# Optimization experiments

Hardware: AMD Instinct MI355X
Metric: run time of the kernel (lower is better)

## Reference

```python
import jax, jax.numpy as jnp
import numpy as np

NUM_HEADS = 8
ATTN_LEN = 5


def setup_inputs() -> dict:
    rng = jax.random.key(0)
    ks = jax.random.split(rng, 10)
    B, T, D = 2, 4096, 1024
    H, HD = NUM_HEADS, D // NUM_HEADS
    n = lambda k, shape, scale=1.0: jax.random.normal(k, shape, jnp.float32) * scale
    return {
        "query": n(ks[0], (B, T, D)),
        "key": n(ks[1], (B, T, D)),
        "value": n(ks[2], (B, T, D)),
        "Wq": n(ks[3], (D, D), 0.02),
        "bq": jnp.zeros((D,), jnp.float32),
        "Wk": n(ks[4], (D, D), 0.02),
        "bk": jnp.zeros((D,), jnp.float32),
        "Wv": n(ks[5], (D, D), 0.02),
        "bv": jnp.zeros((D,), jnp.float32),
        "Er": n(ks[6], (H, HD, ATTN_LEN)),
        "layer": 1,
    }


def _forward(query, key, value, Wq, bq, Wk, bk, Wv, bv, Er, layer):
    B, T, D = query.shape
    H = NUM_HEADS
    HD = D // H
    dil = 2 ** layer
    pad = dil * (ATTN_LEN // 2)
    Tp = T + 2 * pad

    # torch nn.Linear: y = x @ W^T + b ; reshape to [B, H, T, HD]
    q = (query @ Wq.T + bq).reshape(B, T, H, HD).transpose(0, 2, 1, 3)
    k = (key @ Wk.T + bk).reshape(B, T, H, HD).transpose(0, 2, 1, 3)
    v = (value @ Wv.T + bv).reshape(B, T, H, HD).transpose(0, 2, 1, 3)

    # head-group source mapping + shifts (note k head 7 reuses k head 6, per source)
    src_k = jnp.array([0, 1, 2, 3, 4, 5, 6, 6])
    src_v = jnp.array([0, 1, 2, 3, 4, 5, 6, 7])
    shifts = jnp.array([0, 0, 0, 0, -2, -1, 1, 2])

    # kv_roll equivalence: window slot j at time t for shift s reads
    # padded[(t + (s + j) * dil) mod Tp]  (torch.roll wraparound included)
    t_idx = jnp.arange(T)
    j_idx = jnp.arange(ATTN_LEN)
    idx = (t_idx[None, :, None] + (shifts[:, None, None] + j_idx[None, None, :]) * dil) % Tp  # [H,T,L]

    def windows(x, src):
        xp = jnp.pad(x, ((0, 0), (0, 0), (pad, pad), (0, 0)))[:, src]  # [B,H,Tp,HD]
        g = jnp.take_along_axis(xp, idx.reshape(1, H, T * ATTN_LEN, 1), axis=2)
        return g.reshape(B, H, T, ATTN_LEN, HD)

    kw = windows(k, src_k)  # [B,H,T,L,HD]
    vw = windows(v, src_v)

    qk = jnp.einsum('bhtd,bhtjd->bhtj', q, kw)            # [B,H,T,L]
    mask = jnp.where(qk == 0.0, -jnp.inf, 0.0)            # zero dot product => padding
    qer = jnp.einsum('bhtd,hdj->bhtj', q, Er)             # relative positional bias
    attn = jax.nn.softmax((qk + qer) / np.sqrt(HD).astype(np.float32) + mask, axis=-1)
    out = jnp.einsum('bhtj,bhtjd->bhtd', attn, vw)        # [B,H,T,HD]
    out = out.transpose(0, 2, 1, 3).reshape(B, T, D)
    return out, attn[:, :, :, None, :]                     # attn shaped [B,H,T,1,L] like torch


def reference(query, key, value, Wq, bq, Wk, bk, Wv, bv, Er, layer):
    return _forward(query, key, value, Wq, bq, Wk, bk, Wv, bv, Er, layer)
```

## Files before the change

kernel.cpp:

```cpp
#include <hip/hip_runtime.h>
#include <hip/hip_bf16.h>

constexpr int B_ = 2, T_ = 4096, D_ = 1024, H_ = 8, HD_ = 128, L_ = 5;
constexpr int M_ = B_ * T_;
constexpr int K_ = D_;
constexpr int N_ = D_;
constexpr int TB_ = 64;
constexpr int NSMAX_ = 96;

typedef __attribute__((ext_vector_type(8))) __bf16 bf16x8;
typedef __attribute__((ext_vector_type(4))) float f32x4;

__device__ __constant__ int c_srck[8]  = {0, 1, 2, 3, 4, 5, 6, 6};
__device__ __constant__ int c_shift[8] = {0, 0, 0, 0, -2, -1, 1, 2};

__device__ __forceinline__ void gload_lds16(const void* g, void* l) {
    __builtin_amdgcn_global_load_lds(
        (__attribute__((address_space(1))) void*)g,
        (__attribute__((address_space(3))) void*)l, 16, 0, 0);
}

__global__ __launch_bounds__(256) void cvt_kernel(
    const float* __restrict__ q,  const float* __restrict__ k,  const float* __restrict__ v,
    const float* __restrict__ wq, const float* __restrict__ wk, const float* __restrict__ wv,
    __hip_bfloat16* __restrict__ qb,  __hip_bfloat16* __restrict__ kb,  __hip_bfloat16* __restrict__ vb,
    __hip_bfloat16* __restrict__ wqb, __hip_bfloat16* __restrict__ wkb, __hip_bfloat16* __restrict__ wvb)
{
    const int y = blockIdx.y;
    const float* src;
    __hip_bfloat16* dst;
    size_t idx;
    if (blockIdx.x < 4096) {
        src = (y == 0) ? q : (y == 1) ? k : v;
        dst = (y == 0) ? qb : (y == 1) ? kb : vb;
        idx = ((size_t)blockIdx.x * 256 + threadIdx.x) * 8;
    } else {
        src = (y == 0) ? wq : (y == 1) ? wk : wv;
        dst = (y == 0) ? wqb : (y == 1) ? wkb : wvb;
        idx = ((size_t)(blockIdx.x - 4096) * 256 + threadIdx.x) * 8;
    }
    f32x4 a = *(const f32x4*)(const void*)(src + idx);
    f32x4 b = *(const f32x4*)(const void*)(src + idx + 4);
    bf16x8 o;
#pragma unroll
    for (int e = 0; e < 4; ++e) { o[e] = (__bf16)a[e]; o[e + 4] = (__bf16)b[e]; }
    *(bf16x8*)(void*)(dst + idx) = o;
}

__global__ __launch_bounds__(256) void qkv_gemm_bf16(
    const __hip_bfloat16* __restrict__ qb,
    const __hip_bfloat16* __restrict__ kb,
    const __hip_bfloat16* __restrict__ vb,
    const __hip_bfloat16* __restrict__ wqb,
    const __hip_bfloat16* __restrict__ wkb,
    const __hip_bfloat16* __restrict__ wvb,
    const float* __restrict__ bq,
    const float* __restrict__ bk,
    const float* __restrict__ bv,
    __hip_bfloat16* __restrict__ qout,
    __hip_bfloat16* __restrict__ kout,
    __hip_bfloat16* __restrict__ vout)
{
    const int z = blockIdx.z;
    const __hip_bfloat16* A = (z == 0) ? qb  : (z == 1) ? kb  : vb;
    const __hip_bfloat16* W = (z == 0) ? wqb : (z == 1) ? wkb : wvb;
    const float* bias       = (z == 0) ? bq  : (z == 1) ? bk  : bv;
    __hip_bfloat16* C       = (z == 0) ? qout : (z == 1) ? kout : vout;

    __shared__ __align__(16) __hip_bfloat16 As[128 * 32];
    __shared__ __align__(16) __hip_bfloat16 Bs[128 * 32];

    const int tid  = threadIdx.x;
    const int wave = tid >> 6;
    const int lane = tid & 63;
    const int m0 = blockIdx.x * 128;
    const int n0 = blockIdx.y * 128;
    const int wm = (wave >> 1) * 64;
    const int wn = (wave & 1) * 64;

    f32x4 acc[4][4];
#pragma unroll
    for (int i = 0; i < 4; ++i)
#pragma unroll
        for (int j = 0; j < 4; ++j)
            acc[i][j] = (f32x4){0.f, 0.f, 0.f, 0.f};

    const int srow = lane >> 2;
    const int scol = (lane & 3) * 8;

    const int fr = lane & 15;
    const int fk = (lane >> 4) * 8;

    for (int k0 = 0; k0 < K_; k0 += 32) {
#pragma unroll
        for (int r = 0; r < 2; ++r) {
            const int issue = wave + r * 4;
            const int row = issue * 16 + srow;
            gload_lds16(A + (size_t)(m0 + row) * K_ + k0 + scol,
                        (void*)(As + issue * 512));
            gload_lds16(W + (size_t)(n0 + row) * K_ + k0 + scol,
                        (void*)(Bs + issue * 512));
        }
        __syncthreads();

        bf16x8 af[4], bf[4];
#pragma unroll
        for (int i = 0; i < 4; ++i) {
            af[i] = *(const bf16x8*)(const void*)(As + (wm + i * 16 + fr) * 32 + fk);
            bf[i] = *(const bf16x8*)(const void*)(Bs + (wn + i * 16 + fr) * 32 + fk);
        }
#pragma unroll
        for (int i = 0; i < 4; ++i)
#pragma unroll
            for (int j = 0; j < 4; ++j)
                acc[i][j] = __builtin_amdgcn_mfma_f32_16x16x32_bf16(
                    af[i], bf[j], acc[i][j], 0, 0, 0);
        __syncthreads();
    }

    const int col_l = lane & 15;
    const int row_l = (lane >> 4) * 4;
#pragma unroll
    for (int j = 0; j < 4; ++j) {
        const int n = n0 + wn + j * 16 + col_l;
        const float bval = bias[n];
#pragma unroll
        for (int i = 0; i < 4; ++i) {
            const int m = m0 + wm + i * 16 + row_l;
#pragma unroll
            for (int r = 0; r < 4; ++r)
                C[(size_t)(m + r) * N_ + n] = __float2bfloat16(acc[i][j][r] + bval);
        }
    }
}

__global__ __launch_bounds__(256) void qkv_gemm_f32(
    const float* __restrict__ query,
    const float* __restrict__ key,
    const float* __restrict__ value,
    const float* __restrict__ Wq,
    const float* __restrict__ bq,
    const float* __restrict__ Wk,
    const float* __restrict__ bk,
    const float* __restrict__ Wv,
    const float* __restrict__ bv,
    __hip_bfloat16* __restrict__ qout,
    __hip_bfloat16* __restrict__ kout,
    __hip_bfloat16* __restrict__ vout)
{
    const int z = blockIdx.z;
    const float* A    = (z == 0) ? query : (z == 1) ? key : value;
    const float* W    = (z == 0) ? Wq    : (z == 1) ? Wk  : Wv;
    const float* bias = (z == 0) ? bq    : (z == 1) ? bk  : bv;
    __hip_bfloat16* C = (z == 0) ? qout  : (z == 1) ? kout : vout;

    __shared__ __align__(16) float As[128 * 32];
    __shared__ __align__(16) float Bs[128 * 32];

    const int tid  = threadIdx.x;
    const int wave = tid >> 6;
    const int lane = tid & 63;
    const int m0 = blockIdx.x * 128;
    const int n0 = blockIdx.y * 128;
    const int wm = (wave >> 1) * 64;
    const int wn = (wave & 1) * 64;

    f32x4 acc[4][4];
#pragma unroll
    for (int i = 0; i < 4; ++i)
#pragma unroll
        for (int j = 0; j < 4; ++j)
            acc[i][j] = (f32x4){0.f, 0.f, 0.f, 0.f};

    const int srow = lane >> 3;
    const int lcg  = (lane & 7) ^ srow;
    const int gcol = lcg * 4;

    const int fr  = lane & 15;
    const int r7  = fr & 7;
    const int cgA = (lane >> 4) * 2;
    const int pcg0 = (cgA)     ^ r7;
    const int pcg1 = (cgA ^ 1) ^ r7;

    for (int k0 = 0; k0 < K_; k0 += 32) {
#pragma unroll
        for (int r = 0; r < 4; ++r) {
            const int issue = wave + r * 4;
            const int row = issue * 8 + srow;
            gload_lds16(A + (size_t)(m0 + row) * K_ + k0 + gcol,
                        (void*)(As + issue * 256));
            gload_lds16(W + (size_t)(n0 + row) * K_ + k0 + gcol,
                        (void*)(Bs + issue * 256));
        }
        __syncthreads();

        bf16x8 af[4], bf[4];
#pragma unroll
        for (int i = 0; i < 4; ++i) {
            const float* ap = As + (wm + i * 16 + fr) * 32;
            f32x4 a0 = *(const f32x4*)(const void*)(ap + pcg0 * 4);
            f32x4 a1 = *(const f32x4*)(const void*)(ap + pcg1 * 4);
            const float* bp = Bs + (wn + i * 16 + fr) * 32;
            f32x4 b0 = *(const f32x4*)(const void*)(bp + pcg0 * 4);
            f32x4 b1 = *(const f32x4*)(const void*)(bp + pcg1 * 4);
#pragma unroll
            for (int e = 0; e < 4; ++e) {
                af[i][e]     = (__bf16)a0[e];
                af[i][e + 4] = (__bf16)a1[e];
                bf[i][e]     = (__bf16)b0[e];
                bf[i][e + 4] = (__bf16)b1[e];
            }
        }
#pragma unroll
        for (int i = 0; i < 4; ++i)
#pragma unroll
            for (int j = 0; j < 4; ++j)
                acc[i][j] = __builtin_amdgcn_mfma_f32_16x16x32_bf16(
                    af[i], bf[j], acc[i][j], 0, 0, 0);
        __syncthreads();
    }

    const int col_l = lane & 15;
    const int row_l = (lane >> 4) * 4;
#pragma unroll
    for (int j = 0; j < 4; ++j) {
        const int n = n0 + wn + j * 16 + col_l;
        const float bval = bias[n];
#pragma unroll
        for (int i = 0; i < 4; ++i) {
            const int m = m0 + wm + i * 16 + row_l;
#pragma unroll
            for (int r = 0; r < 4; ++r)
                C[(size_t)(m + r) * N_ + n] = __float2bfloat16(acc[i][j][r] + bval);
        }
    }
}

__global__ __launch_bounds__(256) void attn_kernel(
    const __hip_bfloat16* __restrict__ qp,
    const __hip_bfloat16* __restrict__ kp,
    const __hip_bfloat16* __restrict__ vp,
    const float* __restrict__ Er,
    const int* __restrict__ layer_p,
    float* __restrict__ out,
    float* __restrict__ attn_out)
{
    const int dil = 1 << (*layer_p);
    int NS = TB_ + 4 * dil;
    if (NS > NSMAX_) NS = NSMAX_;

    const int tid = threadIdx.x;
    const int t0 = blockIdx.x * TB_;
    const int h  = blockIdx.y;
    const int b  = blockIdx.z;
    const int shift = c_shift[h];
    const int srck  = c_srck[h];
    const int off_lo = (shift - 2) * dil;

    __shared__ __align__(16) __hip_bfloat16 Ks[NSMAX_ * 128];
    __shared__ __align__(16) float ErT[5][128];

    for (int i = tid; i < 640; i += 256) {
        const int d = i / 5, j = i - d * 5;
        ErT[j][d] = Er[(size_t)h * 640 + i];
    }

    const int sr = tid >> 4;
    const int sc = tid & 15;
    for (int i0 = 0; i0 < NS; i0 += 16) {
        const int i = i0 + sr;
        if (i < NS) {
            const int r = t0 + off_lo + i;
            bf16x8 kv8 = (bf16x8){0, 0, 0, 0, 0, 0, 0, 0};
            if (r >= 0 && r < T_) {
                kv8 = *(const bf16x8*)(const void*)(
                    kp + (size_t)(b * T_ + r) * D_ + srck * HD_ + sc * 8);
            }
            const int pc = sc ^ (i & 3);
            *(bf16x8*)(void*)(Ks + i * 128 + pc * 8) = kv8;
        }
    }

    const int lr = tid >> 2;
    const int ld = tid & 3;
    const int t  = t0 + lr;
    const size_t qoff = (size_t)(b * T_ + t) * D_ + h * HD_ + ld * 32;

    float qf[32];
#pragma unroll
    for (int c = 0; c < 4; ++c) {
        bf16x8 qv = *(const bf16x8*)(const void*)(qp + qoff + c * 8);
#pragma unroll
        for (int e = 0; e < 8; ++e) qf[c * 8 + e] = (float)qv[e];
    }
    __syncthreads();

    float lg[5];
    bool  valid[5];
    int   orig[5];
#pragma unroll
    for (int j = 0; j < 5; ++j) {
        const int i = lr + j * dil;
        orig[j] = t + (shift + j - 2) * dil;
        valid[j] = (orig[j] >= 0) && (orig[j] < T_);

        float s = 0.f;
#pragma unroll
        for (int c = 0; c < 4; ++c) {
            const int pc = (ld * 4 + c) ^ (i & 3);
            bf16x8 kk = *(const bf16x8*)(const void*)(Ks + i * 128 + pc * 8);
#pragma unroll
            for (int e = 0; e < 8; ++e) s += qf[c * 8 + e] * (float)kk[e];
        }
        if (!valid[j]) s = 0.f;
#pragma unroll
        for (int c = 0; c < 8; ++c) {
            f32x4 ev = *(const f32x4*)(const void*)(&ErT[j][ld * 32 + c * 4]);
#pragma unroll
            for (int e = 0; e < 4; ++e) s += qf[c * 4 + e] * ev[e];
        }
        s += __shfl_xor(s, 1, 4);
        s += __shfl_xor(s, 2, 4);
        lg[j] = valid[j] ? s * 0.08838834764831845f : -INFINITY;
    }

    float mx = lg[0];
#pragma unroll
    for (int j = 1; j < 5; ++j) mx = fmaxf(mx, lg[j]);
    float w[5], sum = 0.f;
#pragma unroll
    for (int j = 0; j < 5; ++j) {
        w[j] = valid[j] ? __expf(lg[j] - mx) : 0.f;
        sum += w[j];
    }
    const float inv = 1.f / sum;
#pragma unroll
    for (int j = 0; j < 5; ++j) w[j] *= inv;

    float o[32];
#pragma unroll
    for (int m = 0; m < 32; ++m) o[m] = 0.f;
#pragma unroll
    for (int j = 0; j < 5; ++j) {
        if (valid[j]) {
            const __hip_bfloat16* vrow =
                vp + (size_t)(b * T_ + orig[j]) * D_ + h * HD_ + ld * 32;
#pragma unroll
            for (int c = 0; c < 4; ++c) {
                bf16x8 vv = *(const bf16x8*)(const void*)(vrow + c * 8);
#pragma unroll
                for (int e = 0; e < 8; ++e) o[c * 8 + e] += w[j] * (float)vv[e];
            }
        }
    }

#pragma unroll
    for (int c = 0; c < 8; ++c) {
        f32x4 ov = (f32x4){o[c * 4], o[c * 4 + 1], o[c * 4 + 2], o[c * 4 + 3]};
        *(f32x4*)(void*)(out + qoff + c * 4) = ov;
    }

    const size_t abase = ((size_t)(b * H_ + h) * T_ + t) * L_;
    attn_out[abase + ld] = w[ld];
    if (ld == 0) attn_out[abase + 4] = w[4];
}

extern "C" void kernel_launch(void* const* d_in, const int* in_sizes, int n_in,
                              void* d_out, int out_size, void* d_ws, size_t ws_size,
                              hipStream_t stream) {
    const float* query = (const float*)d_in[0];
    const float* key   = (const float*)d_in[1];
    const float* value = (const float*)d_in[2];
    const float* Wq    = (const float*)d_in[3];
    const float* bq    = (const float*)d_in[4];
    const float* Wk    = (const float*)d_in[5];
    const float* bk    = (const float*)d_in[6];
    const float* Wv    = (const float*)d_in[7];
    const float* bv    = (const float*)d_in[8];
    const float* Er    = (const float*)d_in[9];
    const int*   layer = (const int*)d_in[10];

    float* out  = (float*)d_out;
    float* attn = out + (size_t)B_ * T_ * D_;

    const size_t SA = (size_t)M_ * K_;
    const size_t SW = (size_t)N_ * K_;
    const size_t SP = (size_t)M_ * N_;
    const size_t need = (3 * SA + 3 * SW + 3 * SP) * sizeof(__hip_bfloat16);

    char* ws = (char*)d_ws;
    if (ws_size >= need) {
        __hip_bfloat16* qb  = (__hip_bfloat16*)ws;
        __hip_bfloat16* kb  = qb + SA;
        __hip_bfloat16* vb  = kb + SA;
        __hip_bfloat16* wqb = vb + SA;
        __hip_bfloat16* wkb = wqb + SW;
        __hip_bfloat16* wvb = wkb + SW;
        __hip_bfloat16* qp  = wvb + SW;
        __hip_bfloat16* kp  = qp + SP;
        __hip_bfloat16* vp  = kp + SP;

        cvt_kernel<<<dim3(4608, 3), 256, 0, stream>>>(
            query, key, value, Wq, Wk, Wv, qb, kb, vb, wqb, wkb, wvb);

        qkv_gemm_bf16<<<dim3(M_ / 128, N_ / 128, 3), 256, 0, stream>>>(
            qb, kb, vb, wqb, wkb, wvb, bq, bk, bv, qp, kp, vp);

        attn_kernel<<<dim3(T_ / TB_, H_, B_), 256, 0, stream>>>(
            qp, kp, vp, Er, layer, out, attn);
    } else {
        __hip_bfloat16* qp = (__hip_bfloat16*)ws;
        __hip_bfloat16* kp = qp + SP;
        __hip_bfloat16* vp = kp + SP;

        qkv_gemm_f32<<<dim3(M_ / 128, N_ / 128, 3), 256, 0, stream>>>(
            query, key, value, Wq, bq, Wk, bk, Wv, bv, qp, kp, vp);

        attn_kernel<<<dim3(T_ / TB_, H_, B_), 256, 0, stream>>>(
            qp, kp, vp, Er, layer, out, attn);
    }
}
```

Before: 251.6 us.

## Fuse fp32-to-bf16 activation conversion into QKV GEMM A-tile loads

The separate conversion pass over the query, key and value activations is removed. The GEMM now reads fp32 A tiles straight into registers, converts them to bf16 and writes them to LDS, prefetching the next k-slice into registers. The weight-only conversion kernel remains. This avoids writing and re-reading about 48MB of bf16 activations. In exchange, each A tile is re-read in fp32 once per N-block (8 times), and the A path gives up the direct global-to-LDS loads.

```diff
diff --git a/kernel.cpp b/kernel.cpp
--- a/kernel.cpp
+++ b/kernel.cpp
@@ -20,25 +20,14 @@
         (__attribute__((address_space(3))) void*)l, 16, 0, 0);
 }
 
-__global__ __launch_bounds__(256) void cvt_kernel(
-    const float* __restrict__ q,  const float* __restrict__ k,  const float* __restrict__ v,
+__global__ __launch_bounds__(256) void cvt_w_kernel(
     const float* __restrict__ wq, const float* __restrict__ wk, const float* __restrict__ wv,
-    __hip_bfloat16* __restrict__ qb,  __hip_bfloat16* __restrict__ kb,  __hip_bfloat16* __restrict__ vb,
     __hip_bfloat16* __restrict__ wqb, __hip_bfloat16* __restrict__ wkb, __hip_bfloat16* __restrict__ wvb)
 {
     const int y = blockIdx.y;
-    const float* src;
-    __hip_bfloat16* dst;
-    size_t idx;
-    if (blockIdx.x < 4096) {
-        src = (y == 0) ? q : (y == 1) ? k : v;
-        dst = (y == 0) ? qb : (y == 1) ? kb : vb;
-        idx = ((size_t)blockIdx.x * 256 + threadIdx.x) * 8;
-    } else {
-        src = (y == 0) ? wq : (y == 1) ? wk : wv;
-        dst = (y == 0) ? wqb : (y == 1) ? wkb : wvb;
-        idx = ((size_t)(blockIdx.x - 4096) * 256 + threadIdx.x) * 8;
-    }
+    const float* src = (y == 0) ? wq : (y == 1) ? wk : wv;
+    __hip_bfloat16* dst = (y == 0) ? wqb : (y == 1) ? wkb : wvb;
+    const size_t idx = ((size_t)blockIdx.x * 256 + threadIdx.x) * 8;
     f32x4 a = *(const f32x4*)(const void*)(src + idx);
     f32x4 b = *(const f32x4*)(const void*)(src + idx + 4);
     bf16x8 o;
@@ -47,10 +36,10 @@
     *(bf16x8*)(void*)(dst + idx) = o;
 }
 
-__global__ __launch_bounds__(256) void qkv_gemm_bf16(
-    const __hip_bfloat16* __restrict__ qb,
-    const __hip_bfloat16* __restrict__ kb,
-    const __hip_bfloat16* __restrict__ vb,
+__global__ __launch_bounds__(256) void qkv_gemm_af32(
+    const float* __restrict__ query,
+    const float* __restrict__ key,
+    const float* __restrict__ value,
     const __hip_bfloat16* __restrict__ wqb,
     const __hip_bfloat16* __restrict__ wkb,
     const __hip_bfloat16* __restrict__ wvb,
@@ -62,7 +51,7 @@
     __hip_bfloat16* __restrict__ vout)
 {
     const int z = blockIdx.z;
-    const __hip_bfloat16* A = (z == 0) ? qb  : (z == 1) ? kb  : vb;
+    const float* A          = (z == 0) ? query : (z == 1) ? key : value;
     const __hip_bfloat16* W = (z == 0) ? wqb : (z == 1) ? wkb : wvb;
     const float* bias       = (z == 0) ? bq  : (z == 1) ? bk  : bv;
     __hip_bfloat16* C       = (z == 0) ? qout : (z == 1) ? kout : vout;
@@ -91,17 +80,42 @@
     const int fr = lane & 15;
     const int fk = (lane >> 4) * 8;
 
+    f32x4 rA[2][2];
+    auto loadA = [&](int k0) {
+#pragma unroll
+        for (int r = 0; r < 2; ++r) {
+            const int row = (wave + r * 4) * 16 + srow;
+            const float* pa = A + (size_t)(m0 + row) * K_ + k0 + scol;
+            rA[r][0] = *(const f32x4*)(const void*)pa;
+            rA[r][1] = *(const f32x4*)(const void*)(pa + 4);
+        }
+    };
+    auto writeA = [&]() {
+#pragma unroll
+        for (int r = 0; r < 2; ++r) {
+            bf16x8 oa;
+#pragma unroll
+            for (int e = 0; e < 4; ++e) {
+                oa[e]     = (__bf16)rA[r][0][e];
+                oa[e + 4] = (__bf16)rA[r][1][e];
+            }
+            *(bf16x8*)(void*)(As + (wave + r * 4) * 512 + lane * 8) = oa;
+        }
+    };
+
+    loadA(0);
+
     for (int k0 = 0; k0 < K_; k0 += 32) {
 #pragma unroll
         for (int r = 0; r < 2; ++r) {
             const int issue = wave + r * 4;
-            const int row = issue * 16 + srow;
-            gload_lds16(A + (size_t)(m0 + row) * K_ + k0 + scol,
-                        (void*)(As + issue * 512));
-            gload_lds16(W + (size_t)(n0 + row) * K_ + k0 + scol,
+            gload_lds16(W + (size_t)(n0 + issue * 16 + srow) * K_ + k0 + scol,
                         (void*)(Bs + issue * 512));
         }
+        writeA();
         __syncthreads();
+
+        if (k0 + 32 < K_) loadA(k0 + 32);
 
         bf16x8 af[4], bf[4];
 #pragma unroll
@@ -383,28 +397,24 @@
     float* out  = (float*)d_out;
     float* attn = out + (size_t)B_ * T_ * D_;
 
-    const size_t SA = (size_t)M_ * K_;
     const size_t SW = (size_t)N_ * K_;
     const size_t SP = (size_t)M_ * N_;
-    const size_t need = (3 * SA + 3 * SW + 3 * SP) * sizeof(__hip_bfloat16);
+    const size_t need = (3 * SW + 3 * SP) * sizeof(__hip_bfloat16);
 
     char* ws = (char*)d_ws;
     if (ws_size >= need) {
-        __hip_bfloat16* qb  = (__hip_bfloat16*)ws;
-        __hip_bfloat16* kb  = qb + SA;
-        __hip_bfloat16* vb  = kb + SA;
-        __hip_bfloat16* wqb = vb + SA;
+        __hip_bfloat16* wqb = (__hip_bfloat16*)ws;
         __hip_bfloat16* wkb = wqb + SW;
         __hip_bfloat16* wvb = wkb + SW;
         __hip_bfloat16* qp  = wvb + SW;
         __hip_bfloat16* kp  = qp + SP;
         __hip_bfloat16* vp  = kp + SP;
 
-        cvt_kernel<<<dim3(4608, 3), 256, 0, stream>>>(
-            query, key, value, Wq, Wk, Wv, qb, kb, vb, wqb, wkb, wvb);
-
-        qkv_gemm_bf16<<<dim3(M_ / 128, N_ / 128, 3), 256, 0, stream>>>(
-            qb, kb, vb, wqb, wkb, wvb, bq, bk, bv, qp, kp, vp);
+        cvt_w_kernel<<<dim3(512, 3), 256, 0, stream>>>(
+            Wq, Wk, Wv, wqb, wkb, wvb);
+
+        qkv_gemm_af32<<<dim3(M_ / 128, N_ / 128, 3), 256, 0, stream>>>(
+            query, key, value, wqb, wkb, wvb, bq, bk, bv, qp, kp, vp);
 
         attn_kernel<<<dim3(T_ / TB_, H_, B_), 256, 0, stream>>>(
             qp, kp, vp, Er, layer, out, attn);
```

Result: slower. 258.9 us (+2.9%).
